# Optimization experiments

Hardware: AMD Instinct MI355X
Metric: run time of the kernel (lower is better)

## Reference

```python
import jax, jax.numpy as jnp
import numpy as np


def setup_inputs() -> dict:
    key = jax.random.key(0)
    k1, k2, k3 = jax.random.split(key, 3)
    N, C_in, H, W = 16, 64, 256, 256
    C_out, K = 128, 3
    x = jax.random.normal(k1, (N, C_in, H, W), dtype=jnp.float32)
    # kaiming-ish small init for stability through tanh
    conv_weight = jax.random.normal(k2, (C_out, C_in, K, K), dtype=jnp.float32) * 0.05
    conv_bias = jax.random.normal(k3, (C_out,), dtype=jnp.float32) * 0.05
    return {"x": x, "conv_weight": conv_weight, "conv_bias": conv_bias}


def reference(x, conv_weight, conv_bias):
    # VALID conv, stride 1, NCHW / OIHW (matches the CUDA kernel: H_out = H - K + 1)
    y = jax.lax.conv_general_dilated(
        x, conv_weight,
        window_strides=(1, 1), padding='VALID',
        dimension_numbers=('NCHW', 'OIHW', 'NCHW'))
    y = y + conv_bias[None, :, None, None]
    # fused pattern: double tanh then per-pixel min over output channels (keepdim)
    y = jnp.tanh(jnp.tanh(y))
    out = jnp.min(y, axis=1, keepdims=True)  # (N, 1, H_out, W_out)
    return out
```

## Files before the change

### kernel.cpp

```cpp
#include <hip/hip_runtime.h>
#include <stdint.h>

typedef _Float16 half8 __attribute__((ext_vector_type(8)));
typedef float float4v __attribute__((ext_vector_type(4)));

#define H_IN 256
#define W_IN 256
#define H_OUT 254
#define W_OUT 254
#define T_COLS 68
#define A_ROWS 408
#define A_BYTES (A_ROWS * 128)
#define B_SLAB  8192
#define B_BYTES (3 * B_SLAB)
#define MIN_BYTES (2 * 256 * 4)
#define SMEM_BYTES (A_BYTES + B_BYTES + MIN_BYTES)

__global__ void pack_w_kernel(const float* __restrict__ w, _Float16* __restrict__ Bp3) {
    int idx = blockIdx.x * 256 + threadIdx.x;
    if (idx >= 73728) return;
    int g   = idx >> 12;
    int rem = idx & 4095;
    int co  = rem >> 5;
    int s16 = (rem >> 3) & 3;
    int e   = rem & 7;
    int q   = s16 ^ ((co >> 2) & 3);
    int tap = g >> 1, h = g & 1;
    int cin = h * 32 + q * 8 + e;
    int kh  = tap / 3, kw = tap - kh * 3;
    Bp3[idx] = (_Float16)w[(co * 64 + cin) * 9 + kh * 3 + kw];
}

__device__ __forceinline__ int akey(int row) {
    return (((row & 7) ^ ((row >> 3) & 7)) << 4);
}

__global__ __launch_bounds__(512, 4)
void conv_v8_kernel(const float* __restrict__ x,
                    const _Float16* __restrict__ Bp3,
                    const float* __restrict__ bias,
                    float* __restrict__ out) {
    extern __shared__ __align__(16) char smem[];
    char*  Alds   = smem;
    char*  Blds   = smem + A_BYTES;
    float* minbuf = (float*)(smem + A_BYTES + B_BYTES);

    const int tid  = threadIdx.x;
    const int lane = tid & 63;
    const int wave = tid >> 6;
    const int ow0  = blockIdx.x * 64;
    const int oh0  = blockIdx.y * 4;
    const int nb   = blockIdx.z;
    const int wr   = wave >> 1;
    const int wc   = wave & 1;
    const int q    = lane >> 4;
    const int lr   = lane & 15;

#pragma unroll
    for (int s = 0; s < 2; ++s) {
        const char* src = (const char*)Bp3 + s * B_SLAB + tid * 16;
        char* dstb = Blds + s * B_SLAB + (tid & ~63) * 16;
        __builtin_amdgcn_global_load_lds(
            (const __attribute__((address_space(1))) uint32_t*)src,
            (__attribute__((address_space(3))) uint32_t*)dstb, 16, 0, 0);
    }

    float bv[4];
#pragma unroll
    for (int n = 0; n < 4; ++n) bv[n] = bias[wc * 64 + n * 16 + lr];

    {
        const float* xb = x + (size_t)nb * (64 * H_IN * W_IN);
#pragma unroll
        for (int k = 0; k < 2; ++k) {
            int id = tid + 512 * k;
            if (id < 816) {
                int oct  = (unsigned)id / 102u;
                int pxq  = id - oct * 102;
                int row0 = pxq * 4;
                int r    = (unsigned)row0 / (unsigned)T_COLS;
                int c    = row0 - r * T_COLS;
                int ih   = oh0 + r; if (ih > H_IN - 1) ih = H_IN - 1;
                int iw   = ow0 + c; if (iw > W_IN - 4) iw = W_IN - 4;
                const float* src = xb + (size_t)(oct * 8) * (H_IN * W_IN)
                                      + (size_t)ih * W_IN + iw;
                float4v f[8];
#pragma unroll
                for (int u = 0; u < 8; ++u)
                    f[u] = *(const float4v*)(src + (size_t)u * (H_IN * W_IN));
#pragma unroll
                for (int j = 0; j < 4; ++j) {
                    int row = row0 + j;
                    half8 hv;
#pragma unroll
                    for (int u = 0; u < 8; ++u) hv[u] = (_Float16)f[u][j];
                    *(half8*)(Alds + row * 128 + ((oct * 16) ^ akey(row))) = hv;
                }
            }
        }
    }
    __syncthreads();

    float4v acc[4][4];
#pragma unroll
    for (int m = 0; m < 4; ++m)
#pragma unroll
        for (int n = 0; n < 4; ++n)
#pragma unroll
            for (int i = 0; i < 4; ++i) acc[m][n][i] = 0.0f;

    const int bslot = (q ^ ((lr >> 2) & 3)) << 4;
    const int bco   = (wc * 64 + lr) * 64;

#pragma unroll
    for (int g = 0; g < 18; ++g) {
        if (g < 17) asm volatile("s_waitcnt vmcnt(1)" ::: "memory");
        else        asm volatile("s_waitcnt vmcnt(0)" ::: "memory");
        __builtin_amdgcn_s_barrier();
        __builtin_amdgcn_sched_barrier(0);

        if (g < 16) {
            const char* src = (const char*)Bp3 + (size_t)(g + 2) * B_SLAB + tid * 16;
            char* dstb = Blds + ((g + 2) % 3) * B_SLAB + (tid & ~63) * 16;
            __builtin_amdgcn_global_load_lds(
                (const __attribute__((address_space(1))) uint32_t*)src,
                (__attribute__((address_space(3))) uint32_t*)dstb, 16, 0, 0);
        }

        const int tap = g >> 1, h = g & 1;
        const int kh = tap / 3, kw = tap - kh * 3;
        const int kb = h * 64 + q * 16;

        half8 a[4], b[4];
#pragma unroll
        for (int n = 0; n < 4; ++n)
            b[n] = *(const half8*)(Blds + (g % 3) * B_SLAB + bco + n * 1024 + bslot);
#pragma unroll
        for (int m = 0; m < 4; ++m) {
            int row = (wr + kh) * T_COLS + m * 16 + lr + kw;
            a[m] = *(const half8*)(Alds + row * 128 + (kb ^ akey(row)));
        }

        __builtin_amdgcn_s_setprio(1);
#pragma unroll
        for (int m = 0; m < 4; ++m)
#pragma unroll
            for (int n = 0; n < 4; ++n)
                acc[m][n] = __builtin_amdgcn_mfma_f32_16x16x32_f16(
                    a[m], b[n], acc[m][n], 0, 0, 0);
        __builtin_amdgcn_s_setprio(0);
    }

#pragma unroll
    for (int m = 0; m < 4; ++m) {
        float4v v;
#pragma unroll
        for (int n = 0; n < 4; ++n) {
#pragma unroll
            for (int i = 0; i < 4; ++i) {
                float t = acc[m][n][i] + bv[n];
                v[i] = (n == 0) ? t : fminf(v[i], t);
            }
        }
#pragma unroll
        for (int off = 1; off < 16; off <<= 1)
#pragma unroll
            for (int i = 0; i < 4; ++i)
                v[i] = fminf(v[i], __shfl_xor(v[i], off, 64));
        if (lr == 0) {
#pragma unroll
            for (int i = 0; i < 4; ++i)
                minbuf[wc * 256 + wr * 64 + m * 16 + q * 4 + i] = v[i];
        }
    }
    __syncthreads();

    if (tid < 256) {
        int r = tid >> 6, c = tid & 63;
        int oh = oh0 + r, ow = ow0 + c;
        if (oh < H_OUT && ow < W_OUT) {
            float mv = fminf(minbuf[tid], minbuf[256 + tid]);
            out[((size_t)nb * H_OUT + oh) * W_OUT + ow] = tanhf(tanhf(mv));
        }
    }
}

extern "C" void kernel_launch(void* const* d_in, const int* in_sizes, int n_in,
                              void* d_out, int out_size, void* d_ws, size_t ws_size,
                              hipStream_t stream) {
    const float* x    = (const float*)d_in[0];
    const float* w    = (const float*)d_in[1];
    const float* bias = (const float*)d_in[2];
    float* out        = (float*)d_out;
    _Float16* Bp3     = (_Float16*)d_ws;

    pack_w_kernel<<<dim3(288), dim3(256), 0, stream>>>(w, Bp3);
    conv_v8_kernel<<<dim3(4, 64, 16), dim3(512), SMEM_BYTES, stream>>>(x, Bp3, bias, out);
}
```

Baseline: 168.6 us.

## Halve block to 256 threads, double per-wave M tile, register-staged B double buffer

Block size drops from 512 to 256 threads, so each wave now computes an 8x4 grid of MFMA tiles (two output rows) instead of 4x4. Each A-fragment LDS read then feeds more MFMAs. The B weight pipeline changes from a 3-slab global_load_lds ring to a 2-slab double buffer staged through registers: loads are issued before the MFMAs and written to LDS afterwards, with a barrier each step. This raises accumulator register pressure (128 fp32 acc per lane) and lowers the occupancy target to 2 blocks, in exchange for better reuse and smaller LDS use.

```diff
diff --git a/kernel.cpp b/kernel.cpp
--- a/kernel.cpp
+++ b/kernel.cpp
@@ -3,6 +3,7 @@
 
 typedef _Float16 half8 __attribute__((ext_vector_type(8)));
 typedef float float4v __attribute__((ext_vector_type(4)));
+typedef unsigned int uint4v __attribute__((ext_vector_type(4)));
 
 #define H_IN 256
 #define W_IN 256
@@ -12,7 +13,7 @@
 #define A_ROWS 408
 #define A_BYTES (A_ROWS * 128)
 #define B_SLAB  8192
-#define B_BYTES (3 * B_SLAB)
+#define B_BYTES (2 * B_SLAB)
 #define MIN_BYTES (2 * 256 * 4)
 #define SMEM_BYTES (A_BYTES + B_BYTES + MIN_BYTES)
 
@@ -35,11 +36,11 @@
     return (((row & 7) ^ ((row >> 3) & 7)) << 4);
 }
 
-__global__ __launch_bounds__(512, 4)
-void conv_v8_kernel(const float* __restrict__ x,
-                    const _Float16* __restrict__ Bp3,
-                    const float* __restrict__ bias,
-                    float* __restrict__ out) {
+__global__ __launch_bounds__(256, 2)
+void conv_v12_kernel(const float* __restrict__ x,
+                     const _Float16* __restrict__ Bp3,
+                     const float* __restrict__ bias,
+                     float* __restrict__ out) {
     extern __shared__ __align__(16) char smem[];
     char*  Alds   = smem;
     char*  Blds   = smem + A_BYTES;
@@ -56,32 +57,24 @@
     const int q    = lane >> 4;
     const int lr   = lane & 15;
 
-#pragma unroll
-    for (int s = 0; s < 2; ++s) {
-        const char* src = (const char*)Bp3 + s * B_SLAB + tid * 16;
-        char* dstb = Blds + s * B_SLAB + (tid & ~63) * 16;
-        __builtin_amdgcn_global_load_lds(
-            (const __attribute__((address_space(1))) uint32_t*)src,
-            (__attribute__((address_space(3))) uint32_t*)dstb, 16, 0, 0);
-    }
-
-    float bv[4];
-#pragma unroll
-    for (int n = 0; n < 4; ++n) bv[n] = bias[wc * 64 + n * 16 + lr];
+    const uint4v* bsrc = (const uint4v*)Bp3;
+
+    uint4v breg0 = bsrc[tid];
+    uint4v breg1 = bsrc[tid + 256];
 
     {
         const float* xb = x + (size_t)nb * (64 * H_IN * W_IN);
 #pragma unroll
-        for (int k = 0; k < 2; ++k) {
-            int id = tid + 512 * k;
+        for (int k = 0; k < 4; ++k) {
+            int id = tid + 256 * k;
             if (id < 816) {
-                int oct  = (unsigned)id / 102u;
-                int pxq  = id - oct * 102;
-                int row0 = pxq * 4;
-                int r    = (unsigned)row0 / (unsigned)T_COLS;
-                int c    = row0 - r * T_COLS;
+                int pxq = id >> 3;
+                int oct = id & 7;
+                int r   = (unsigned)pxq / 17u;
+                int q4  = pxq - r * 17;
+                int row0 = r * T_COLS + q4 * 4;
                 int ih   = oh0 + r; if (ih > H_IN - 1) ih = H_IN - 1;
-                int iw   = ow0 + c; if (iw > W_IN - 4) iw = W_IN - 4;
+                int iw   = ow0 + q4 * 4; if (iw > W_IN - 4) iw = W_IN - 4;
                 const float* src = xb + (size_t)(oct * 8) * (H_IN * W_IN)
                                       + (size_t)ih * W_IN + iw;
                 float4v f[8];
@@ -99,60 +92,68 @@
             }
         }
     }
+    *(uint4v*)(Blds + tid * 16)         = breg0;
+    *(uint4v*)(Blds + (tid + 256) * 16) = breg1;
     __syncthreads();
 
-    float4v acc[4][4];
-#pragma unroll
-    for (int m = 0; m < 4; ++m)
-#pragma unroll
-        for (int n = 0; n < 4; ++n)
-#pragma unroll
-            for (int i = 0; i < 4; ++i) acc[m][n][i] = 0.0f;
+    float bv[4];
+#pragma unroll
+    for (int n = 0; n < 4; ++n) bv[n] = bias[wc * 64 + n * 16 + lr];
 
     const int bslot = (q ^ ((lr >> 2) & 3)) << 4;
     const int bco   = (wc * 64 + lr) * 64;
 
+    float4v acc[8][4];
+#pragma unroll
+    for (int m = 0; m < 8; ++m)
+#pragma unroll
+        for (int n = 0; n < 4; ++n)
+#pragma unroll
+            for (int i = 0; i < 4; ++i) acc[m][n][i] = 0.0f;
+
 #pragma unroll
     for (int g = 0; g < 18; ++g) {
-        if (g < 17) asm volatile("s_waitcnt vmcnt(1)" ::: "memory");
-        else        asm volatile("s_waitcnt vmcnt(0)" ::: "memory");
-        __builtin_amdgcn_s_barrier();
-        __builtin_amdgcn_sched_barrier(0);
-
-        if (g < 16) {
-            const char* src = (const char*)Bp3 + (size_t)(g + 2) * B_SLAB + tid * 16;
-            char* dstb = Blds + ((g + 2) % 3) * B_SLAB + (tid & ~63) * 16;
-            __builtin_amdgcn_global_load_lds(
-                (const __attribute__((address_space(1))) uint32_t*)src,
-                (__attribute__((address_space(3))) uint32_t*)dstb, 16, 0, 0);
+        if (g < 17) {
+            breg0 = bsrc[(g + 1) * 512 + tid];
+            breg1 = bsrc[(g + 1) * 512 + tid + 256];
+            __builtin_amdgcn_sched_barrier(0);
         }
 
         const int tap = g >> 1, h = g & 1;
         const int kh = tap / 3, kw = tap - kh * 3;
         const int kb = h * 64 + q * 16;
-
-        half8 a[4], b[4];
+        const char* slab = Blds + (g & 1) * B_SLAB;
+
+        half8 a[8], b[4];
 #pragma unroll
         for (int n = 0; n < 4; ++n)
-            b[n] = *(const half8*)(Blds + (g % 3) * B_SLAB + bco + n * 1024 + bslot);
-#pragma unroll
-        for (int m = 0; m < 4; ++m) {
-            int row = (wr + kh) * T_COLS + m * 16 + lr + kw;
+            b[n] = *(const half8*)(slab + bco + n * 1024 + bslot);
+#pragma unroll
+        for (int m = 0; m < 8; ++m) {
+            int row = (wr * 2 + (m >> 2) + kh) * T_COLS + (m & 3) * 16 + lr + kw;
             a[m] = *(const half8*)(Alds + row * 128 + (kb ^ akey(row)));
         }
 
         __builtin_amdgcn_s_setprio(1);
 #pragma unroll
-        for (int m = 0; m < 4; ++m)
+        for (int m = 0; m < 8; ++m)
 #pragma unroll
             for (int n = 0; n < 4; ++n)
                 acc[m][n] = __builtin_amdgcn_mfma_f32_16x16x32_f16(
                     a[m], b[n], acc[m][n], 0, 0, 0);
         __builtin_amdgcn_s_setprio(0);
-    }
-
-#pragma unroll
-    for (int m = 0; m < 4; ++m) {
+
+        if (g < 17) {
+            char* dst = Blds + ((g + 1) & 1) * B_SLAB;
+            *(uint4v*)(dst + tid * 16)         = breg0;
+            *(uint4v*)(dst + (tid + 256) * 16) = breg1;
+        }
+        asm volatile("s_waitcnt lgkmcnt(0)" ::: "memory");
+        __builtin_amdgcn_s_barrier();
+    }
+
+#pragma unroll
+    for (int m = 0; m < 8; ++m) {
         float4v v;
 #pragma unroll
         for (int n = 0; n < 4; ++n) {
@@ -170,12 +171,12 @@
         if (lr == 0) {
 #pragma unroll
             for (int i = 0; i < 4; ++i)
-                minbuf[wc * 256 + wr * 64 + m * 16 + q * 4 + i] = v[i];
+                minbuf[wc * 256 + wr * 128 + m * 16 + q * 4 + i] = v[i];
         }
     }
     __syncthreads();
 
-    if (tid < 256) {
+    {
         int r = tid >> 6, c = tid & 63;
         int oh = oh0 + r, ow = ow0 + c;
         if (oh < H_OUT && ow < W_OUT) {
@@ -195,5 +196,5 @@
     _Float16* Bp3     = (_Float16*)d_ws;
 
     pack_w_kernel<<<dim3(288), dim3(256), 0, stream>>>(w, Bp3);
-    conv_v8_kernel<<<dim3(4, 64, 16), dim3(512), SMEM_BYTES, stream>>>(x, Bp3, bias, out);
-}
+    conv_v12_kernel<<<dim3(4, 64, 16), dim3(256), SMEM_BYTES, stream>>>(x, Bp3, bias, out);
+}
```

Measured after the change: 189.3 us. +12.2%, slower.
